# Performance work log

Hardware: AMD Instinct MI355X
Metric: run time of the kernel (lower is better)

The kernel has to match this reference:

```python
import jax, jax.numpy as jnp
import numpy as np
from jax import lax

B, CIN, T, H, K, E = 128, 64, 2048, 128, 9, 600000
N = B * T  # nodes after view
NEG_SLOPE = 0.2
EPS_BN = 1e-5

def setup_inputs() -> dict:
    key = jax.random.key(0)
    ks = jax.random.split(key, 14)
    s = 0.05
    return {
        "x": jax.random.normal(ks[0], (B, CIN, T), jnp.float32),
        "edge_index": jax.random.randint(ks[1], (2, E), 0, N, dtype=jnp.int64),
        "conv1_w": jax.random.normal(ks[2], (H, CIN, K), jnp.float32) * s,
        "conv1_b": jax.random.normal(ks[3], (H,), jnp.float32) * s,
        "Wl": jax.random.normal(ks[4], (H, H), jnp.float32) * s,
        "bl": jax.random.normal(ks[5], (H,), jnp.float32) * s,
        "Wr": jax.random.normal(ks[6], (H, H), jnp.float32) * s,
        "br": jax.random.normal(ks[7], (H,), jnp.float32) * s,
        "att": jax.random.normal(ks[8], (H,), jnp.float32) * s,
        "gat_bias": jax.random.normal(ks[9], (H,), jnp.float32) * s,
        "bn_gamma": jnp.ones((H,), jnp.float32),
        "bn_beta": jnp.zeros((H,), jnp.float32),
        "conv2_w": jax.random.normal(ks[10], (H, H, K), jnp.float32) * s,
        "conv2_b": jax.random.normal(ks[11], (H,), jnp.float32) * s,
    }

def _conv1d_same(x, w, b):
    # x: [B, C, T], w: [O, C, K]
    y = lax.conv_general_dilated(x, w, (1,), 'SAME', dimension_numbers=('NCH', 'OIH', 'NCH'))
    return y + b[None, :, None]

def reference(x, edge_index, conv1_w, conv1_b, Wl, bl, Wr, br, att, gat_bias, bn_gamma, bn_beta, conv2_w, conv2_b):
    b, _, t = x.shape
    h = jax.nn.relu(_conv1d_same(x, conv1_w, conv1_b))          # [B, H, T]
    n_feat = h.reshape(t * b, h.shape[1])                        # torch .view on contiguous [B,H,T]
    n = n_feat.shape[0]
    # GATv2Conv, heads=1, add_self_loops=True
    loops = jnp.arange(n, dtype=edge_index.dtype)
    src = jnp.concatenate([edge_index[0], loops])                # message source j
    dst = jnp.concatenate([edge_index[1], loops])                # target i
    xl = n_feat @ Wl.T + bl                                      # [N, H]
    xr = n_feat @ Wr.T + br
    e = jax.nn.leaky_relu(xl[src] + xr[dst], NEG_SLOPE) @ att    # [Etot]
    m = jax.ops.segment_max(e, dst, num_segments=n)
    a = jnp.exp(e - m[dst])
    denom = jax.ops.segment_sum(a, dst, num_segments=n)
    alpha = a / (denom[dst] + 1e-16)
    out = jax.ops.segment_sum(alpha[:, None] * xl[src], dst, num_segments=n) + gat_bias
    out = jax.nn.relu(out)
    # BatchNorm1d (training mode: batch stats, biased var)
    mu = out.mean(0)
    var = out.var(0)
    out = (out - mu) / jnp.sqrt(var + EPS_BN) * bn_gamma + bn_beta
    out = out.reshape(b, out.shape[1], t)                        # [B, H, T]
    return jax.nn.relu(_conv1d_same(out, conv2_w, conv2_b))
```

## Files before the change

kernel.cpp:

```cpp
#include <hip/hip_runtime.h>

#define NB    128
#define NCIN  64
#define NT    2048
#define HD    128
#define NK    9
#define NE    600000
#define NNODE (NB*NT)
#define NTOT  (NE + NNODE)
static const size_t NELEM = (size_t)NNODE * HD;

typedef unsigned int u32;
typedef unsigned short ushort_t;
typedef __attribute__((ext_vector_type(8))) short short8;
typedef __attribute__((ext_vector_type(4))) float f32x4;

__device__ __forceinline__ ushort_t f2b(float f) {
  u32 x = __float_as_uint(f);
  return (ushort_t)((x + 0x7fffu + ((x >> 16) & 1u)) >> 16);
}

__global__ __launch_bounds__(256) void detect_edges(const int* __restrict__ ebuf,
                                                    int* __restrict__ flag) {
  __shared__ int s;
  if (threadIdx.x == 0) s = 0;
  __syncthreads();
  int any = 0;
  for (int i = threadIdx.x; i < 512; i += 256)
    if (ebuf[2 * i + 1] != 0) any = 1;
  if (any) atomicOr(&s, 1);
  __syncthreads();
  if (threadIdx.x == 0) *flag = s;
}

__global__ __launch_bounds__(256) void convert_edges(const int* __restrict__ ebuf,
                                                     const int* __restrict__ flag,
                                                     int* __restrict__ out) {
  int i = blockIdx.x * 256 + threadIdx.x;
  if (i >= 2 * NE) return;
  out[i] = (*flag) ? ebuf[i] : ebuf[2 * i];
}

__global__ __launch_bounds__(256) void conv_w_prep(const float* __restrict__ w,
                                                   ushort_t* __restrict__ wt,
                                                   int CI) {
  int idx = blockIdx.x * 256 + threadIdx.x;
  if (idx >= NK * HD * CI) return;
  const int ci = idx % CI;
  const int o  = (idx / CI) % HD;
  const int k  = idx / (CI * HD);
  wt[idx] = f2b(w[(o * CI + ci) * NK + k]);
}

__global__ __launch_bounds__(256) void wlr_prep(const float* __restrict__ Wl,
                                                const float* __restrict__ Wr,
                                                ushort_t* __restrict__ wb) {
  int i = blockIdx.x * 256 + threadIdx.x;
  if (i >= HD * HD) return;
  wb[i] = f2b(Wl[i]);
  wb[HD * HD + i] = f2b(Wr[i]);
}

template<int CI, bool AFFINE>
__global__ __launch_bounds__(256) void conv_mfma(
    const float* __restrict__ xin, const ushort_t* __restrict__ wtb,
    const float* __restrict__ bias, const float* __restrict__ scale,
    const float* __restrict__ shift, float* __restrict__ outp)
{
  constexpr int LDSW = CI + 8;
  constexpr int L2CI = (CI == 64) ? 6 : 7;
  const int t0 = blockIdx.x * 64;
  const int b  = blockIdx.y;
  __shared__ __align__(16) ushort_t xs[72 * LDSW];

  const int tid = threadIdx.x;
  const float* xb = xin + (size_t)b * CI * NT;

  for (int u = tid; u < CI * 18; u += 256) {
    const int ci = u & (CI - 1);
    const int tq = u >> L2CI;
    const int gt = t0 - 4 + tq * 4;
    float4 v = make_float4(0.f, 0.f, 0.f, 0.f);
    const float* src = xb + (size_t)ci * NT + gt;
    if (gt >= 0 && gt + 3 < NT) {
      v = *reinterpret_cast<const float4*>(src);
    } else {
      float* vp = &v.x;
      #pragma unroll
      for (int e = 0; e < 4; ++e) {
        const int g = gt + e;
        if (g >= 0 && g < NT) vp[e] = src[e];
      }
    }
    float* vp = &v.x;
    #pragma unroll
    for (int e = 0; e < 4; ++e) {
      float val = vp[e];
      if (AFFINE) {
        const int g = gt + e;
        if (g >= 0 && g < NT) val = val * scale[g & 127] + shift[g & 127];
      }
      xs[(tq * 4 + e) * LDSW + ci] = f2b(val);
    }
  }
  __syncthreads();

  const int lane = tid & 63;
  const int wid  = tid >> 6;
  const int wo   = wid >> 1;
  const int wt   = wid & 1;
  const int l15  = lane & 15;
  const int lk   = lane >> 4;

  f32x4 acc[4][2];
  #pragma unroll
  for (int mr = 0; mr < 4; ++mr)
    #pragma unroll
    for (int nr = 0; nr < 2; ++nr) acc[mr][nr] = (f32x4){0.f, 0.f, 0.f, 0.f};

  const ushort_t* wbase = wtb + (size_t)(wo * 64 + l15) * CI + lk * 8;

  for (int k = 0; k < NK; ++k) {
    const ushort_t* wk = wbase + (size_t)k * HD * CI;
    #pragma unroll
    for (int cc = 0; cc < CI / 32; ++cc) {
      short8 bfr[2];
      #pragma unroll
      for (int nr = 0; nr < 2; ++nr)
        bfr[nr] = *reinterpret_cast<const short8*>(
            &xs[(wt * 32 + nr * 16 + l15 + k) * LDSW + cc * 32 + lk * 8]);
      #pragma unroll
      for (int mr = 0; mr < 4; ++mr) {
        const short8 afr = *reinterpret_cast<const short8*>(wk + mr * 16 * CI + cc * 32);
        #pragma unroll
        for (int nr = 0; nr < 2; ++nr)
          acc[mr][nr] = __builtin_amdgcn_mfma_f32_16x16x32_bf16(afr, bfr[nr], acc[mr][nr], 0, 0, 0);
      }
    }
  }

  const int tcol = t0 + wt * 32 + l15;
  #pragma unroll
  for (int mr = 0; mr < 4; ++mr) {
    #pragma unroll
    for (int e = 0; e < 4; ++e) {
      const int o = wo * 64 + mr * 16 + lk * 4 + e;
      const float bv = bias[o];
      float* orow = outp + ((size_t)b * HD + o) * NT;
      #pragma unroll
      for (int nr = 0; nr < 2; ++nr) {
        float v = acc[mr][nr][e] + bv;
        orow[tcol + nr * 16] = v > 0.f ? v : 0.f;
      }
    }
  }
}

__global__ __launch_bounds__(256) void gemm_xlxr_mfma(
    const float* __restrict__ nf, const ushort_t* __restrict__ wb,
    const float* __restrict__ bl, const float* __restrict__ br,
    float* __restrict__ xl, float* __restrict__ xr)
{
  const int n0 = blockIdx.x * 64;
  __shared__ __align__(16) ushort_t nfs[64 * 136];
  const int tid = threadIdx.x;

  for (int u = tid; u < 64 * 16; u += 256) {
    const int r = u >> 4, c8 = (u & 15) * 8;
    const float* src = nf + (size_t)(n0 + r) * HD + c8;
    const float4 v0 = *reinterpret_cast<const float4*>(src);
    const float4 v1 = *reinterpret_cast<const float4*>(src + 4);
    ushort_t tmp[8] = {f2b(v0.x), f2b(v0.y), f2b(v0.z), f2b(v0.w),
                       f2b(v1.x), f2b(v1.y), f2b(v1.z), f2b(v1.w)};
    *reinterpret_cast<short8*>(&nfs[r * 136 + c8]) = *reinterpret_cast<const short8*>(tmp);
  }
  __syncthreads();

  const int lane = tid & 63;
  const int wid  = tid >> 6;
  const int l15  = lane & 15;
  const int lk   = lane >> 4;

  f32x4 accl[8], accr[8];
  #pragma unroll
  for (int nt = 0; nt < 8; ++nt) {
    accl[nt] = (f32x4){0.f, 0.f, 0.f, 0.f};
    accr[nt] = (f32x4){0.f, 0.f, 0.f, 0.f};
  }

  #pragma unroll
  for (int kc = 0; kc < 4; ++kc) {
    const short8 afr = *reinterpret_cast<const short8*>(
        &nfs[(wid * 16 + l15) * 136 + kc * 32 + lk * 8]);
    const ushort_t* wrow = wb + (size_t)l15 * HD + kc * 32 + lk * 8;
    #pragma unroll
    for (int nt = 0; nt < 8; ++nt) {
      const short8 bfl = *reinterpret_cast<const short8*>(wrow + nt * 16 * HD);
      const short8 bfr = *reinterpret_cast<const short8*>(wrow + HD * HD + nt * 16 * HD);
      accl[nt] = __builtin_amdgcn_mfma_f32_16x16x32_bf16(afr, bfl, accl[nt], 0, 0, 0);
      accr[nt] = __builtin_amdgcn_mfma_f32_16x16x32_bf16(afr, bfr, accr[nt], 0, 0, 0);
    }
  }

  #pragma unroll
  for (int nt = 0; nt < 8; ++nt) {
    const int feat = nt * 16 + l15;
    const float bvl = bl[feat], bvr = br[feat];
    #pragma unroll
    for (int e = 0; e < 4; ++e) {
      const size_t row = (size_t)(n0 + wid * 16 + lk * 4 + e) * HD;
      xl[row + feat] = accl[nt][e] + bvl;
      xr[row + feat] = accr[nt][e] + bvr;
    }
  }
}

__global__ __launch_bounds__(256) void csr_count(const int* __restrict__ esrc,
                                                 const int* __restrict__ edst,
                                                 u32* __restrict__ cnt) {
  const int eid = blockIdx.x * 256 + threadIdx.x;
  if (eid >= NTOT) return;
  const int d = (eid < NE) ? edst[eid] : eid - NE;
  atomicAdd(&cnt[d], 1u);
}

__global__ __launch_bounds__(256) void scan1(const u32* __restrict__ cnt,
                                             u32* __restrict__ rs,
                                             u32* __restrict__ bsum) {
  __shared__ u32 tmp[256];
  const int t = threadIdx.x;
  const int i = blockIdx.x * 256 + t;
  const u32 v = cnt[i];
  tmp[t] = v;
  __syncthreads();
  for (int off = 1; off < 256; off <<= 1) {
    const u32 a = (t >= off) ? tmp[t - off] : 0u;
    __syncthreads();
    tmp[t] += a;
    __syncthreads();
  }
  rs[i] = tmp[t] - v;
  if (t == 255) bsum[blockIdx.x] = tmp[255];
}

__global__ __launch_bounds__(1024) void scan2(u32* __restrict__ bsum) {
  __shared__ u32 tmp[1024];
  const int t = threadIdx.x;
  const u32 v = bsum[t];
  tmp[t] = v;
  __syncthreads();
  for (int off = 1; off < 1024; off <<= 1) {
    const u32 a = (t >= off) ? tmp[t - off] : 0u;
    __syncthreads();
    tmp[t] += a;
    __syncthreads();
  }
  bsum[t] = tmp[t] - v;
}

__global__ __launch_bounds__(256) void scan3(u32* __restrict__ rs,
                                             const u32* __restrict__ bsum,
                                             u32* __restrict__ pos) {
  const int i = blockIdx.x * 256 + threadIdx.x;
  const u32 r = rs[i] + bsum[blockIdx.x];
  rs[i] = r;
  pos[i] = r;
}

__global__ __launch_bounds__(256) void csr_scatter(const int* __restrict__ esrc,
                                                   const int* __restrict__ edst,
                                                   u32* __restrict__ pos,
                                                   int* __restrict__ csr) {
  const int eid = blockIdx.x * 256 + threadIdx.x;
  if (eid >= NTOT) return;
  int s_, d_;
  if (eid < NE) { s_ = esrc[eid]; d_ = edst[eid]; } else { s_ = d_ = eid - NE; }
  const u32 p = atomicAdd(&pos[d_], 1u);
  csr[p] = s_;
}

__global__ __launch_bounds__(256) void gat_fused(
    const int* __restrict__ csr, const u32* __restrict__ rs,
    const u32* __restrict__ cnt, const float* __restrict__ xl,
    float* __restrict__ xrout, const float* __restrict__ att,
    const float* __restrict__ gbias, float* __restrict__ stats)
{
  __shared__ float sacc[2][128];
  const int tid = threadIdx.x;
  if (tid < 128) { sacc[0][tid] = 0.f; sacc[1][tid] = 0.f; }
  __syncthreads();
  const int lane = tid & 63;
  const int wid  = tid >> 6;
  const float attl = att[lane], atth = att[lane + 64];
  const float gbl = gbias[lane], gbh = gbias[lane + 64];
  float s1l = 0.f, s2l = 0.f, s1h = 0.f, s2h = 0.f;
  const int dbase = blockIdx.x * 64 + wid * 16;

  for (int i = 0; i < 16; ++i) {
    const int d = dbase + i;
    float* xrow = xrout + (size_t)d * HD;
    const float xrl = xrow[lane], xrh = xrow[lane + 64];
    const u32 start = rs[d];
    const u32 deg = cnt[d];
    float m = -INFINITY, s = 0.f, accl = 0.f, acch = 0.f;
    for (u32 j = 0; j < deg; ++j) {
      const int src = csr[start + j];
      const float* xls = xl + (size_t)src * HD;
      const float xll = xls[lane], xlh = xls[lane + 64];
      float q0 = xll + xrl; q0 = q0 > 0.f ? q0 : 0.2f * q0;
      float q1 = xlh + xrh; q1 = q1 > 0.f ? q1 : 0.2f * q1;
      float v = attl * q0 + atth * q1;
      #pragma unroll
      for (int off = 32; off > 0; off >>= 1) v += __shfl_xor(v, off);
      const float nm = fmaxf(m, v);
      const float sc = expf(m - nm);
      const float w  = expf(v - nm);
      s = s * sc + w;
      accl = accl * sc + w * xll;
      acch = acch * sc + w * xlh;
      m = nm;
    }
    const float inv = 1.f / (s + 1e-16f);
    float o0 = accl * inv + gbl; o0 = o0 > 0.f ? o0 : 0.f;
    float o1 = acch * inv + gbh; o1 = o1 > 0.f ? o1 : 0.f;
    xrow[lane] = o0;
    xrow[lane + 64] = o1;
    s1l += o0; s2l += o0 * o0;
    s1h += o1; s2h += o1 * o1;
  }

  atomicAdd(&sacc[0][lane], s1l); atomicAdd(&sacc[0][lane + 64], s1h);
  atomicAdd(&sacc[1][lane], s2l); atomicAdd(&sacc[1][lane + 64], s2h);
  __syncthreads();
  atomicAdd(stats + tid, sacc[tid >> 7][tid & 127]);
}

__global__ void bn_params(const float* __restrict__ stats, const float* __restrict__ gamma,
                          const float* __restrict__ beta, float* __restrict__ scsh)
{
  const int f = threadIdx.x;
  const float inv_n = 1.f / (float)NNODE;
  const float mu  = stats[f] * inv_n;
  const float var = stats[HD + f] * inv_n - mu * mu;
  const float sc  = gamma[f] * rsqrtf(var + 1e-5f);
  scsh[f] = sc;
  scsh[HD + f] = beta[f] - mu * sc;
}

extern "C" void kernel_launch(void* const* d_in, const int* in_sizes, int n_in,
                              void* d_out, int out_size, void* d_ws, size_t ws_size,
                              hipStream_t stream) {
  const float* x        = (const float*)d_in[0];
  const int*   edge_raw = (const int*)  d_in[1];
  const float* conv1_w  = (const float*)d_in[2];
  const float* conv1_b  = (const float*)d_in[3];
  const float* Wl       = (const float*)d_in[4];
  const float* bl       = (const float*)d_in[5];
  const float* Wr       = (const float*)d_in[6];
  const float* br       = (const float*)d_in[7];
  const float* att      = (const float*)d_in[8];
  const float* gat_bias = (const float*)d_in[9];
  const float* bn_gamma = (const float*)d_in[10];
  const float* bn_beta  = (const float*)d_in[11];
  const float* conv2_w  = (const float*)d_in[12];
  const float* conv2_b  = (const float*)d_in[13];
  float* out = (float*)d_out;
  char*  ws  = (char*)d_ws;

  const size_t o_xl   = 0;
  const size_t o_xr   = o_xl  + NELEM * 4;
  const size_t o_csr  = o_xr  + NELEM * 4;
  const size_t o_cnt  = o_csr + (size_t)NTOT * 4;
  const size_t o_rs   = o_cnt + (size_t)NNODE * 4;
  const size_t o_pos  = o_rs  + (size_t)NNODE * 4;
  const size_t o_bs   = o_pos + (size_t)NNODE * 4;
  const size_t o_st   = o_bs  + 1024 * 4;
  const size_t o_ed   = o_st  + 4 * HD * 4;
  const size_t o_flag = o_ed  + (size_t)2 * NE * 4;
  const size_t o_w1   = (o_flag + 64) & ~(size_t)63;
  const size_t o_w2   = o_w1 + (size_t)NK * HD * NCIN * 2;
  const size_t o_wlr  = o_w2 + (size_t)NK * HD * HD * 2;

  float* h     = out;
  float* xl    = (float*)(ws + o_xl);
  float* xr    = (float*)(ws + o_xr);
  int*   csr   = (int*)  (ws + o_csr);
  u32*   cnt   = (u32*)  (ws + o_cnt);
  u32*   rs    = (u32*)  (ws + o_rs);
  u32*   pos   = (u32*)  (ws + o_pos);
  u32*   bsum  = (u32*)  (ws + o_bs);
  float* stats = (float*)(ws + o_st);
  int*   ei32  = (int*)  (ws + o_ed);
  int*   flag  = (int*)  (ws + o_flag);
  ushort_t* w1b  = (ushort_t*)(ws + o_w1);
  ushort_t* w2b  = (ushort_t*)(ws + o_w2);
  ushort_t* wlrb = (ushort_t*)(ws + o_wlr);

  hipMemsetAsync(cnt,   0, (size_t)NNODE * 4, stream);
  hipMemsetAsync(stats, 0, 2 * HD * 4, stream);

  detect_edges<<<1, 256, 0, stream>>>(edge_raw, flag);
  convert_edges<<<(2 * NE + 255) / 256, 256, 0, stream>>>(edge_raw, flag, ei32);

  conv_w_prep<<<(NK * HD * NCIN + 255) / 256, 256, 0, stream>>>(conv1_w, w1b, NCIN);
  conv_w_prep<<<(NK * HD * HD + 255) / 256, 256, 0, stream>>>(conv2_w, w2b, HD);
  wlr_prep<<<(HD * HD + 255) / 256, 256, 0, stream>>>(Wl, Wr, wlrb);

  csr_count<<<(NTOT + 255) / 256, 256, 0, stream>>>(ei32, ei32 + NE, cnt);
  scan1<<<NNODE / 256, 256, 0, stream>>>(cnt, rs, bsum);
  scan2<<<1, 1024, 0, stream>>>(bsum);
  scan3<<<NNODE / 256, 256, 0, stream>>>(rs, bsum, pos);
  csr_scatter<<<(NTOT + 255) / 256, 256, 0, stream>>>(ei32, ei32 + NE, pos, csr);

  conv_mfma<NCIN, false><<<dim3(NT / 64, NB), 256, 0, stream>>>(
      x, w1b, conv1_b, nullptr, nullptr, h);

  gemm_xlxr_mfma<<<NNODE / 64, 256, 0, stream>>>(h, wlrb, bl, br, xl, xr);

  gat_fused<<<NNODE / 64, 256, 0, stream>>>(csr, rs, cnt, xl, xr, att, gat_bias, stats);

  bn_params<<<1, HD, 0, stream>>>(stats, bn_gamma, bn_beta, stats + 2 * HD);

  conv_mfma<HD, true><<<dim3(NT / 64, NB), 256, 0, stream>>>(
      xr, w2b, conv2_b, stats + 2 * HD, stats + 3 * HD, out);
}
```

Baseline: 1.172 ms.

## Widen conv MFMA time tile to 128 and prefetch weight fragments

```diff
diff --git a/kernel.cpp b/kernel.cpp
--- a/kernel.cpp
+++ b/kernel.cpp
@@ -68,39 +68,49 @@
     const float* __restrict__ shift, float* __restrict__ outp)
 {
   constexpr int LDSW = CI + 8;
-  constexpr int L2CI = (CI == 64) ? 6 : 7;
-  const int t0 = blockIdx.x * 64;
+  constexpr int NCC  = CI / 32;
+  constexpr int NIDX = NK * NCC;
+  const int t0 = blockIdx.x * 128;
   const int b  = blockIdx.y;
-  __shared__ __align__(16) ushort_t xs[72 * LDSW];
+  __shared__ __align__(16) ushort_t xs[136 * LDSW];
+  __shared__ float sc_s[128], sh_s[128];
 
   const int tid = threadIdx.x;
   const float* xb = xin + (size_t)b * CI * NT;
 
-  for (int u = tid; u < CI * 18; u += 256) {
-    const int ci = u & (CI - 1);
-    const int tq = u >> L2CI;
-    const int gt = t0 - 4 + tq * 4;
-    float4 v = make_float4(0.f, 0.f, 0.f, 0.f);
-    const float* src = xb + (size_t)ci * NT + gt;
-    if (gt >= 0 && gt + 3 < NT) {
-      v = *reinterpret_cast<const float4*>(src);
-    } else {
-      float* vp = &v.x;
-      #pragma unroll
-      for (int e = 0; e < 4; ++e) {
-        const int g = gt + e;
-        if (g >= 0 && g < NT) vp[e] = src[e];
-      }
-    }
-    float* vp = &v.x;
+  if (AFFINE) {
+    if (tid < 128) { sc_s[tid] = scale[tid]; sh_s[tid] = shift[tid]; }
+    __syncthreads();
+  }
+
+  for (int u = tid; u < CI * 32; u += 256) {
+    const int ci = u >> 5;
+    const int qt = u & 31;
+    const int gt = t0 + qt * 4;
+    const float4 v = *reinterpret_cast<const float4*>(xb + (size_t)ci * NT + gt);
+    const float* vp = &v.x;
     #pragma unroll
     for (int e = 0; e < 4; ++e) {
       float val = vp[e];
-      if (AFFINE) {
-        const int g = gt + e;
-        if (g >= 0 && g < NT) val = val * scale[g & 127] + shift[g & 127];
+      if (AFFINE) { const int g = (gt + e) & 127; val = val * sc_s[g] + sh_s[g]; }
+      xs[(qt * 4 + e + 4) * LDSW + ci] = f2b(val);
+    }
+  }
+  for (int u = tid; u < CI * 2; u += 256) {
+    const int ci = u >> 1;
+    const int side = u & 1;
+    const int gt = side ? (t0 + 128) : (t0 - 4);
+    const int rbase = side ? 132 : 0;
+    const float* src = xb + (size_t)ci * NT + gt;
+    #pragma unroll
+    for (int e = 0; e < 4; ++e) {
+      const int g = gt + e;
+      float val = 0.f;
+      if (g >= 0 && g < NT) {
+        val = src[e];
+        if (AFFINE) { const int gg = g & 127; val = val * sc_s[gg] + sh_s[gg]; }
       }
-      xs[(tq * 4 + e) * LDSW + ci] = f2b(val);
+      xs[(rbase + e) * LDSW + ci] = f2b(val);
     }
   }
   __syncthreads();
@@ -112,34 +122,45 @@
   const int l15  = lane & 15;
   const int lk   = lane >> 4;
 
-  f32x4 acc[4][2];
+  f32x4 acc[4][4];
   #pragma unroll
   for (int mr = 0; mr < 4; ++mr)
     #pragma unroll
-    for (int nr = 0; nr < 2; ++nr) acc[mr][nr] = (f32x4){0.f, 0.f, 0.f, 0.f};
+    for (int nr = 0; nr < 4; ++nr) acc[mr][nr] = (f32x4){0.f, 0.f, 0.f, 0.f};
 
   const ushort_t* wbase = wtb + (size_t)(wo * 64 + l15) * CI + lk * 8;
 
-  for (int k = 0; k < NK; ++k) {
-    const ushort_t* wk = wbase + (size_t)k * HD * CI;
-    #pragma unroll
-    for (int cc = 0; cc < CI / 32; ++cc) {
-      short8 bfr[2];
+  short8 a_cur[4], a_nxt[4];
+  #pragma unroll
+  for (int mr = 0; mr < 4; ++mr)
+    a_cur[mr] = *reinterpret_cast<const short8*>(wbase + (size_t)mr * 16 * CI);
+
+  for (int idx = 0; idx < NIDX; ++idx) {
+    const int k  = idx / NCC;
+    const int cc = idx % NCC;
+    const int ni = idx + 1;
+    if (ni < NIDX) {
+      const int k2 = ni / NCC, c2 = ni % NCC;
+      const ushort_t* wn = wbase + ((size_t)k2 * HD) * CI + c2 * 32;
       #pragma unroll
-      for (int nr = 0; nr < 2; ++nr)
-        bfr[nr] = *reinterpret_cast<const short8*>(
-            &xs[(wt * 32 + nr * 16 + l15 + k) * LDSW + cc * 32 + lk * 8]);
+      for (int mr = 0; mr < 4; ++mr)
+        a_nxt[mr] = *reinterpret_cast<const short8*>(wn + (size_t)mr * 16 * CI);
+    }
+    short8 bfr[4];
+    #pragma unroll
+    for (int nr = 0; nr < 4; ++nr)
+      bfr[nr] = *reinterpret_cast<const short8*>(
+          &xs[(wt * 64 + nr * 16 + l15 + k) * LDSW + cc * 32 + lk * 8]);
+    #pragma unroll
+    for (int mr = 0; mr < 4; ++mr)
       #pragma unroll
-      for (int mr = 0; mr < 4; ++mr) {
-        const short8 afr = *reinterpret_cast<const short8*>(wk + mr * 16 * CI + cc * 32);
-        #pragma unroll
-        for (int nr = 0; nr < 2; ++nr)
-          acc[mr][nr] = __builtin_amdgcn_mfma_f32_16x16x32_bf16(afr, bfr[nr], acc[mr][nr], 0, 0, 0);
-      }
-    }
-  }
-
-  const int tcol = t0 + wt * 32 + l15;
+      for (int nr = 0; nr < 4; ++nr)
+        acc[mr][nr] = __builtin_amdgcn_mfma_f32_16x16x32_bf16(a_cur[mr], bfr[nr], acc[mr][nr], 0, 0, 0);
+    #pragma unroll
+    for (int mr = 0; mr < 4; ++mr) a_cur[mr] = a_nxt[mr];
+  }
+
+  const int tcol = t0 + wt * 64 + l15;
   #pragma unroll
   for (int mr = 0; mr < 4; ++mr) {
     #pragma unroll
@@ -148,7 +169,7 @@
       const float bv = bias[o];
       float* orow = outp + ((size_t)b * HD + o) * NT;
       #pragma unroll
-      for (int nr = 0; nr < 2; ++nr) {
+      for (int nr = 0; nr < 4; ++nr) {
         float v = acc[mr][nr][e] + bv;
         orow[tcol + nr * 16] = v > 0.f ? v : 0.f;
       }
@@ -412,7 +433,7 @@
   scan3<<<NNODE / 256, 256, 0, stream>>>(rs, bsum, pos);
   csr_scatter<<<(NTOT + 255) / 256, 256, 0, stream>>>(ei32, ei32 + NE, pos, csr);
 
-  conv_mfma<NCIN, false><<<dim3(NT / 64, NB), 256, 0, stream>>>(
+  conv_mfma<NCIN, false><<<dim3(NT / 128, NB), 256, 0, stream>>>(
       x, w1b, conv1_b, nullptr, nullptr, h);
 
   gemm_xlxr_mfma<<<NNODE / 64, 256, 0, stream>>>(h, wlrb, bl, br, xl, xr);
@@ -421,6 +442,6 @@
 
   bn_params<<<1, HD, 0, stream>>>(stats, bn_gamma, bn_beta, stats + 2 * HD);
 
-  conv_mfma<HD, true><<<dim3(NT / 64, NB), 256, 0, stream>>>(
+  conv_mfma<HD, true><<<dim3(NT / 128, NB), 256, 0, stream>>>(
       xr, w2b, conv2_b, stats + 2 * HD, stats + 3 * HD, out);
 }
```

Result: faster. 976.3 us (-16.7%).
